# Optimization experiments

Measured on AMD Instinct MI355X. Metric: run time of the kernel, lower is better.

The kernel has to match this reference:

```python
import jax, jax.numpy as jnp
import numpy as np

B, S, D = 4, 2048, 1024
H, HK = 16, 4          # num_heads, num_heads_kv
HD = D // H            # head_dim = 64
G = H // HK            # kv groups = 4


def setup_inputs() -> dict:
    key = jax.random.key(0)
    ks = jax.random.split(key, 7)
    s = 0.02
    return {
        "query": jax.random.normal(ks[0], (B, S, D), jnp.float32),
        "key":   jax.random.normal(ks[1], (B, S, D), jnp.float32),
        "value": jax.random.normal(ks[2], (B, S, D), jnp.float32),
        # weights stored (in, out); equivalent to torch Linear y = x @ W.T
        "Wq": jax.random.normal(ks[3], (D, H * HD), jnp.float32) * s,
        "Wk": jax.random.normal(ks[4], (D, HK * HD), jnp.float32) * s,
        "Wv": jax.random.normal(ks[5], (D, HK * HD), jnp.float32) * s,
        "Wo": jax.random.normal(ks[6], (H * HD, D), jnp.float32) * s,
    }


def reference(query, key, value, Wq, Wk, Wv, Wo):
    b, qlen, _ = query.shape
    kvlen = key.shape[1]
    # projections
    q = (query @ Wq).reshape(b, qlen, H, HD)        # [b,q,H,hd]
    k = (key @ Wk).reshape(b, kvlen, HK, HD)        # [b,s,HK,hd]
    v = (value @ Wv).reshape(b, kvlen, HK, HD)      # [b,s,HK,hd]
    # GQA: q head h attends kv head h//G (repeat_interleave semantics)
    qg = q.reshape(b, qlen, HK, G, HD)              # head = kv*G + group
    scale = 1.0 / jnp.sqrt(jnp.asarray(HD, q.dtype))
    # scores [b,HK,G,q,s] -- broadcast kv heads, no materialized repeat
    scores = jnp.einsum('bqkgd,bskd->bkgqs', qg, k) * scale
    attn = jax.nn.softmax(scores, axis=-1)
    out = jnp.einsum('bkgqs,bskd->bqkgd', attn, v)  # [b,q,HK,G,hd]
    out = out.reshape(b, qlen, H * HD)
    return out @ Wo
```

## Files before the change

kernel.cpp:

```cpp
#include <hip/hip_runtime.h>


typedef unsigned short u16;
typedef unsigned int   u32;
typedef __bf16 bf16x4 __attribute__((ext_vector_type(4)));
typedef __bf16 bf16x8 __attribute__((ext_vector_type(8)));
typedef float  f32x4  __attribute__((ext_vector_type(4)));

#define MFMA(a,b,c) __builtin_amdgcn_mfma_f32_16x16x32_bf16((a),(b),(c),0,0,0)

#define GLDS(g, l) __builtin_amdgcn_global_load_lds(                          \
    (const __attribute__((address_space(1))) void*)(g),                       \
    (__attribute__((address_space(3))) void*)(l), 16, 0, 0)

#if __has_builtin(__builtin_amdgcn_exp2f)
#define EXP2(x) __builtin_amdgcn_exp2f(x)
#else
#define EXP2(x) exp2f(x)
#endif

__device__ __forceinline__ u16 f2bf(float f){
    u32 u = __builtin_bit_cast(u32, f);
    u += 0x7fffu + ((u >> 16) & 1u);
    return (u16)(u >> 16);
}
__device__ __forceinline__ u32 pk2(float a, float b){
#if __has_builtin(__builtin_amdgcn_cvt_pk_bf16_f32)
    auto r = __builtin_amdgcn_cvt_pk_bf16_f32(a, b);
    return __builtin_bit_cast(u32, r);
#else
    return (u32)f2bf(a) | ((u32)f2bf(b) << 16);
#endif
}
__device__ __forceinline__ bf16x8 ldfrag(const u16* p){
    return *(const bf16x8*)p;
}
__device__ __forceinline__ bf16x8 ld2x64(const u16* p){
    bf16x4 lo = *(const bf16x4*)p;
    bf16x4 hi = *(const bf16x4*)(p + 4);
    bf16x8 r;
    r[0]=lo[0]; r[1]=lo[1]; r[2]=lo[2]; r[3]=lo[3];
    r[4]=hi[0]; r[5]=hi[1]; r[6]=hi[2]; r[7]=hi[3];
    return r;
}

__global__ __launch_bounds__(256) void prep(const float* __restrict__ q,
                                            const float* __restrict__ k,
                                            const float* __restrict__ v,
                                            const float* __restrict__ Wq,
                                            const float* __restrict__ Wk,
                                            const float* __restrict__ Wv,
                                            const float* __restrict__ Wo,
                                            u16* Qc, u16* Kc, u16* Vc,
                                            u16* WqT, u16* WkT, u16* WvT, u16* WoT){
    const int tid = threadIdx.x, bid = blockIdx.x;
    if (bid < 2560){
        __shared__ float T[32][33];
        const float* W; u16* WT; int N, i;
        if (bid < 1024)      { W = Wq; WT = WqT; N = 1024; i = bid; }
        else if (bid < 1280) { W = Wk; WT = WkT; N =  256; i = bid - 1024; }
        else if (bid < 1536) { W = Wv; WT = WvT; N =  256; i = bid - 1280; }
        else                 { W = Wo; WT = WoT; N = 1024; i = bid - 1536; }
        int kt = (i & 31) * 32, nt = (i >> 5) * 32;
        int r = tid >> 3, c = tid & 7;
        float4 vv = *(const float4*)(W + (size_t)(kt + r) * N + nt + c * 4);
        T[r][c*4+0] = vv.x; T[r][c*4+1] = vv.y; T[r][c*4+2] = vv.z; T[r][c*4+3] = vv.w;
        __syncthreads();
        u32 lo = pk2(T[c*4+0][r], T[c*4+1][r]);
        u32 hi = pk2(T[c*4+2][r], T[c*4+3][r]);
        *(uint2*)(WT + (size_t)(nt + r) * 1024 + kt + c * 4) = make_uint2(lo, hi);
    } else {
        int i = bid - 2560;
        const float* src = (i < 512) ? q : (i < 1024 ? k : v);
        u16*         dst = (i < 512) ? Qc : (i < 1024 ? Kc : Vc);
        size_t off = (size_t)(i & 511) * 16384;
        const float* s = src + off;
        u16* d = dst + off;
        #pragma unroll
        for (int p = 0; p < 16; ++p){
            int idx = (p * 256 + tid) * 4;
            float4 vv = *(const float4*)(s + idx);
            *(uint2*)(d + idx) = make_uint2(pk2(vv.x, vv.y), pk2(vv.z, vv.w));
        }
    }
}

template<int EPI>
__device__ __forceinline__ void gemm_body(const u16* __restrict__ A,
                                          const u16* __restrict__ Bt,
                                          void* __restrict__ Cp,
                                          int N, int K, int m0, int n0,
                                          u16* As, u16* Bs, float oscale){
    const int tid  = threadIdx.x;
    const int wave = tid >> 6, lane = tid & 63;
    const int quad = lane >> 4, l15 = lane & 15;
    const int wm = wave >> 1, wn = wave & 1;
    const int srow = lane >> 3;
    const int scol = ((lane & 7) ^ srow) * 8;
    const int swz  = l15 & 7;

    f32x4 acc[4][4];
    #pragma unroll
    for (int i = 0; i < 4; ++i)
        #pragma unroll
        for (int j = 0; j < 4; ++j) acc[i][j] = (f32x4){0.f, 0.f, 0.f, 0.f};

    const int nkt = K >> 6;
    for (int kt = 0; kt < nkt; ++kt){
        __syncthreads();
        {
            const u16* ga = A + (size_t)(m0 + wave*32 + srow) * K + kt*64 + scol;
            u16* la = As + (wave*32) * 64;
            #pragma unroll
            for (int p = 0; p < 4; ++p)
                GLDS(ga + (size_t)(p*8) * K, la + p*8*64);
            const u16* gb = Bt + (size_t)(n0 + wave*32 + srow) * K + kt*64 + scol;
            u16* lb = Bs + (wave*32) * 64;
            #pragma unroll
            for (int p = 0; p < 4; ++p)
                GLDS(gb + (size_t)(p*8) * K, lb + p*8*64);
        }
        __syncthreads();
        #pragma unroll
        for (int ks = 0; ks < 2; ++ks){
            bf16x8 af[4], bfr[4];
            #pragma unroll
            for (int mt = 0; mt < 4; ++mt)
                af[mt] = ldfrag(&As[(wm*64 + mt*16 + l15) * 64 +
                                    (((ks*4 + quad) ^ swz) * 8)]);
            #pragma unroll
            for (int nt = 0; nt < 4; ++nt)
                bfr[nt] = ldfrag(&Bs[(wn*64 + nt*16 + l15) * 64 +
                                     (((ks*4 + quad) ^ swz) * 8)]);
            #pragma unroll
            for (int mt = 0; mt < 4; ++mt)
                #pragma unroll
                for (int nt = 0; nt < 4; ++nt){
                    if constexpr (EPI == 1)
                        acc[mt][nt] = MFMA(af[mt], bfr[nt], acc[mt][nt]);
                    else
                        acc[mt][nt] = MFMA(bfr[nt], af[mt], acc[mt][nt]);
                }
        }
    }
    #pragma unroll
    for (int mt = 0; mt < 4; ++mt){
        #pragma unroll
        for (int nt = 0; nt < 4; ++nt){
            if constexpr (EPI == 1){
                int rowb = m0 + wm*64 + mt*16 + quad*4;
                int col  = n0 + wn*64 + nt*16 + l15;
                u16* C = (u16*)Cp;
                int bb = rowb >> 11, s = rowb & 2047;
                u32 lo = pk2(acc[mt][nt][0], acc[mt][nt][1]);
                u32 hi = pk2(acc[mt][nt][2], acc[mt][nt][3]);
                *(uint2*)(C + (size_t)(bb * 256 + col) * 2048 + s) = make_uint2(lo, hi);
            } else {
                int row  = m0 + wm*64 + mt*16 + l15;
                int colb = n0 + wn*64 + nt*16 + quad*4;
                if constexpr (EPI == 0){
                    u16* C = (u16*)Cp;
                    u32 lo = pk2(acc[mt][nt][0]*oscale, acc[mt][nt][1]*oscale);
                    u32 hi = pk2(acc[mt][nt][2]*oscale, acc[mt][nt][3]*oscale);
                    *(uint2*)(C + (size_t)row * N + colb) = make_uint2(lo, hi);
                } else {
                    float* C = (float*)Cp;
                    *(f32x4*)(C + (size_t)row * N + colb) = acc[mt][nt];
                }
            }
        }
    }
}

__global__ __launch_bounds__(256) void gemm_qkv(const u16* Qc, const u16* WqT, u16* Qp,
                                                const u16* Kc, const u16* WkT, u16* Kp,
                                                const u16* Vc, const u16* WvT, u16* Vt,
                                                float qscale){
    __shared__ u16 As[128 * 64];
    __shared__ u16 Bs[128 * 64];
    int bid = blockIdx.x;
    if (bid < 512)
        gemm_body<0>(Qc, WqT, Qp, 1024, 1024, (bid >> 3) * 128, (bid & 7) * 128,
                     As, Bs, qscale);
    else if (bid < 640){
        int i = bid - 512;
        gemm_body<0>(Kc, WkT, Kp, 256, 1024, (i >> 1) * 128, (i & 1) * 128,
                     As, Bs, 1.0f);
    } else {
        int i = bid - 640;
        gemm_body<1>(Vc, WvT, Vt, 256, 1024, (i >> 1) * 128, (i & 1) * 128,
                     As, Bs, 1.0f);
    }
}

__global__ __launch_bounds__(256) void gemm_o(const u16* AO, const u16* WoT,
                                              float* Out){
    __shared__ u16 As[128 * 64];
    __shared__ u16 Bs[128 * 64];
    int bid = blockIdx.x;
    gemm_body<2>(AO, WoT, Out, 1024, 1024, (bid >> 3) * 128, (bid & 7) * 128,
                 As, Bs, 1.0f);
}

__global__ __launch_bounds__(512) void attn_k(const u16* __restrict__ Qp,
                                              const u16* __restrict__ Kp,
                                              const u16* __restrict__ Vt,
                                              u16* __restrict__ AO){
    constexpr int S = 2048, Dm = 1024, NKV = 256, PST = 88;
    __shared__ u16 Kb[2][64 * 64];
    __shared__ u16 Vb[2][64 * 64];
    __shared__ u16 Ps[128 * PST];
    const int tid = threadIdx.x, wave = tid >> 6, lane = tid & 63;
    const int quad = lane >> 4, l15 = lane & 15;
    const int qt = blockIdx.x, h = blockIdx.y, b = blockIdx.z;
    const int hk = h >> 2, q0 = qt * 128;
    u16* pw = Ps + wave * (16 * PST);

    const int srow = lane >> 3;
    const int scol = ((lane & 7) ^ srow) * 8;
    const int swz  = l15 & 7;

    auto issue = [&](int t){
        int j0 = t * 64, bufi = t & 1;
        int r = wave * 8 + srow;
        GLDS(Kp + (size_t)(b * S + j0 + r) * NKV + hk * 64 + scol,
             &Kb[bufi][wave * 8 * 64]);
        GLDS(Vt + (size_t)(b * NKV + hk * 64 + r) * S + j0 + scol,
             &Vb[bufi][wave * 8 * 64]);
    };

    issue(0);
    {
        int c8 = tid & 7, r0 = tid >> 3;
        #pragma unroll
        for (int p = 0; p < 2; ++p){
            int r = r0 + p * 64;
            uint4 v = *(const uint4*)(Qp + (size_t)(b * S + q0 + r) * Dm + h * 64 + c8 * 8);
            *(uint2*)&Ps[r * PST + c8 * 8]     = make_uint2(v.x, v.y);
            *(uint2*)&Ps[r * PST + c8 * 8 + 4] = make_uint2(v.z, v.w);
        }
    }
    __syncthreads();
    bf16x8 qf[2];
    #pragma unroll
    for (int ks = 0; ks < 2; ++ks)
        qf[ks] = ld2x64(&Ps[(wave*16 + l15) * PST + ks*32 + quad*8]);

    const u32 one2 = 0x3F803F80u;
    const bf16x8 ones = __builtin_bit_cast(bf16x8, make_uint4(one2, one2, one2, one2));

    f32x4 O[4];
    #pragma unroll
    for (int dt = 0; dt < 4; ++dt) O[dt] = (f32x4){0.f, 0.f, 0.f, 0.f};
    f32x4 sums = (f32x4){0.f, 0.f, 0.f, 0.f};

    for (int t = 0; t < 32; ++t){
        __syncthreads();
        if (t < 31) issue(t + 1);
        const u16* Kt = Kb[t & 1];
        const u16* Vs = Vb[t & 1];
        f32x4 sf[4];
        #pragma unroll
        for (int nt = 0; nt < 4; ++nt) sf[nt] = (f32x4){0.f, 0.f, 0.f, 0.f};
        #pragma unroll
        for (int ks = 0; ks < 2; ++ks){
            #pragma unroll
            for (int nt = 0; nt < 4; ++nt){
                bf16x8 ak = ldfrag(&Kt[(nt*16 + l15) * 64 + (((ks*4 + quad) ^ swz) * 8)]);
                sf[nt] = MFMA(ak, qf[ks], sf[nt]);
            }
        }
        #pragma unroll
        for (int nt = 0; nt < 4; ++nt){
            float e0 = EXP2(sf[nt][0]);
            float e1 = EXP2(sf[nt][1]);
            float e2 = EXP2(sf[nt][2]);
            float e3 = EXP2(sf[nt][3]);
            *(uint2*)&pw[l15 * PST + nt*16 + quad*4] =
                make_uint2(pk2(e0, e1), pk2(e2, e3));
        }
        __threadfence_block();
        #pragma unroll
        for (int ks = 0; ks < 2; ++ks){
            bf16x8 bp = ld2x64(&pw[l15 * PST + ks*32 + quad*8]);
            sums = MFMA(ones, bp, sums);
            #pragma unroll
            for (int dt = 0; dt < 4; ++dt){
                bf16x8 av = ldfrag(&Vs[(dt*16 + l15) * 64 + (((ks*4 + quad) ^ swz) * 8)]);
                O[dt] = MFMA(av, bp, O[dt]);
            }
        }
    }
    float inv = 1.0f / sums[0];
    size_t row = (size_t)(b * S + q0 + wave*16 + l15);
    #pragma unroll
    for (int dt = 0; dt < 4; ++dt){
        u32 lo = pk2(O[dt][0] * inv, O[dt][1] * inv);
        u32 hi = pk2(O[dt][2] * inv, O[dt][3] * inv);
        *(uint2*)(AO + row * Dm + h * 64 + dt*16 + quad*4) = make_uint2(lo, hi);
    }
}

extern "C" void kernel_launch(void* const* d_in, const int* in_sizes, int n_in,
                              void* d_out, int out_size, void* d_ws, size_t ws_size,
                              hipStream_t stream){
    const float* q  = (const float*)d_in[0];
    const float* k  = (const float*)d_in[1];
    const float* v  = (const float*)d_in[2];
    const float* Wq = (const float*)d_in[3];
    const float* Wk = (const float*)d_in[4];
    const float* Wv = (const float*)d_in[5];
    const float* Wo = (const float*)d_in[6];
    char* ws = (char*)d_ws;
    const size_t MB = 1u << 20;
    u16* WqT = (u16*)(ws);
    u16* WkT = (u16*)(ws + 2*MB);
    u16* WvT = (u16*)(ws + 2*MB + 512*1024);
    u16* WoT = (u16*)(ws + 3*MB);
    u16* Qc  = (u16*)(ws + 5*MB);
    u16* Kc  = (u16*)(ws + 21*MB);
    u16* Vc  = (u16*)(ws + 37*MB);
    u16* Qp  = (u16*)(ws + 53*MB);
    u16* Kp  = (u16*)(ws + 69*MB);
    u16* Vt  = (u16*)(ws + 73*MB);
    u16* AO  = (u16*)(ws + 5*MB);

    const float cexp = 0.125f * 1.44269504f;

    prep<<<dim3(4096), 256, 0, stream>>>(q, k, v, Wq, Wk, Wv, Wo,
                                         Qc, Kc, Vc, WqT, WkT, WvT, WoT);
    gemm_qkv<<<dim3(768), 256, 0, stream>>>(Qc, WqT, Qp, Kc, WkT, Kp,
                                            Vc, WvT, Vt, cexp);
    attn_k<<<dim3(16, 16, 4), 512, 0, stream>>>(Qp, Kp, Vt, AO);
    gemm_o<<<dim3(512), 256, 0, stream>>>(AO, WoT, (float*)d_out);
}
```

Before: 320.8 us.

## Give each attention wave four query row-tiles to reuse K/V fragments

```diff
diff --git a/kernel.cpp b/kernel.cpp
--- a/kernel.cpp
+++ b/kernel.cpp
@@ -202,19 +202,19 @@
                  As, Bs, 1.0f);
 }
 
-__global__ __launch_bounds__(512) void attn_k(const u16* __restrict__ Qp,
+__global__ __launch_bounds__(256) void attn_k(const u16* __restrict__ Qp,
                                               const u16* __restrict__ Kp,
                                               const u16* __restrict__ Vt,
                                               u16* __restrict__ AO){
-    constexpr int S = 2048, Dm = 1024, NKV = 256, PST = 88;
+    constexpr int S = 2048, Dm = 1024, NKV = 256, PST = 68;
     __shared__ u16 Kb[2][64 * 64];
     __shared__ u16 Vb[2][64 * 64];
-    __shared__ u16 Ps[128 * PST];
+    __shared__ u16 Ps[256 * PST];
     const int tid = threadIdx.x, wave = tid >> 6, lane = tid & 63;
     const int quad = lane >> 4, l15 = lane & 15;
-    const int qt = blockIdx.x, h = blockIdx.y, b = blockIdx.z;
-    const int hk = h >> 2, q0 = qt * 128;
-    u16* pw = Ps + wave * (16 * PST);
+    const int h = blockIdx.y, b = blockIdx.z;
+    const int hk = h >> 2, q0 = blockIdx.x * 256;
+    u16* pw = Ps + wave * (64 * PST);
 
     const int srow = lane >> 3;
     const int scol = ((lane & 7) ^ srow) * 8;
@@ -222,82 +222,108 @@
 
     auto issue = [&](int t){
         int j0 = t * 64, bufi = t & 1;
-        int r = wave * 8 + srow;
-        GLDS(Kp + (size_t)(b * S + j0 + r) * NKV + hk * 64 + scol,
-             &Kb[bufi][wave * 8 * 64]);
-        GLDS(Vt + (size_t)(b * NKV + hk * 64 + r) * S + j0 + scol,
-             &Vb[bufi][wave * 8 * 64]);
+        #pragma unroll
+        for (int p = 0; p < 2; ++p){
+            int r = wave * 16 + p * 8 + srow;
+            GLDS(Kp + (size_t)(b * S + j0 + r) * NKV + hk * 64 + scol,
+                 &Kb[bufi][(wave * 16 + p * 8) * 64]);
+            GLDS(Vt + (size_t)(b * NKV + hk * 64 + r) * S + j0 + scol,
+                 &Vb[bufi][(wave * 16 + p * 8) * 64]);
+        }
     };
 
     issue(0);
     {
         int c8 = tid & 7, r0 = tid >> 3;
         #pragma unroll
-        for (int p = 0; p < 2; ++p){
-            int r = r0 + p * 64;
+        for (int p = 0; p < 8; ++p){
+            int r = r0 + p * 32;
             uint4 v = *(const uint4*)(Qp + (size_t)(b * S + q0 + r) * Dm + h * 64 + c8 * 8);
             *(uint2*)&Ps[r * PST + c8 * 8]     = make_uint2(v.x, v.y);
             *(uint2*)&Ps[r * PST + c8 * 8 + 4] = make_uint2(v.z, v.w);
         }
     }
     __syncthreads();
-    bf16x8 qf[2];
-    #pragma unroll
-    for (int ks = 0; ks < 2; ++ks)
-        qf[ks] = ld2x64(&Ps[(wave*16 + l15) * PST + ks*32 + quad*8]);
+    bf16x8 qf[4][2];
+    #pragma unroll
+    for (int mt = 0; mt < 4; ++mt)
+        #pragma unroll
+        for (int ks = 0; ks < 2; ++ks)
+            qf[mt][ks] = ld2x64(&Ps[(wave*64 + mt*16 + l15) * PST + ks*32 + quad*8]);
 
     const u32 one2 = 0x3F803F80u;
     const bf16x8 ones = __builtin_bit_cast(bf16x8, make_uint4(one2, one2, one2, one2));
 
-    f32x4 O[4];
-    #pragma unroll
-    for (int dt = 0; dt < 4; ++dt) O[dt] = (f32x4){0.f, 0.f, 0.f, 0.f};
-    f32x4 sums = (f32x4){0.f, 0.f, 0.f, 0.f};
+    f32x4 O[4][4];
+    #pragma unroll
+    for (int dt = 0; dt < 4; ++dt)
+        #pragma unroll
+        for (int mt = 0; mt < 4; ++mt) O[dt][mt] = (f32x4){0.f, 0.f, 0.f, 0.f};
+    f32x4 sums[4];
+    #pragma unroll
+    for (int mt = 0; mt < 4; ++mt) sums[mt] = (f32x4){0.f, 0.f, 0.f, 0.f};
 
     for (int t = 0; t < 32; ++t){
         __syncthreads();
         if (t < 31) issue(t + 1);
         const u16* Kt = Kb[t & 1];
         const u16* Vs = Vb[t & 1];
-        f32x4 sf[4];
-        #pragma unroll
-        for (int nt = 0; nt < 4; ++nt) sf[nt] = (f32x4){0.f, 0.f, 0.f, 0.f};
+        bf16x8 ak[2][4];
+        #pragma unroll
+        for (int ks = 0; ks < 2; ++ks)
+            #pragma unroll
+            for (int nt = 0; nt < 4; ++nt)
+                ak[ks][nt] = ldfrag(&Kt[(nt*16 + l15) * 64 + (((ks*4 + quad) ^ swz) * 8)]);
+        #pragma unroll
+        for (int mt = 0; mt < 4; ++mt){
+            f32x4 sf[4];
+            #pragma unroll
+            for (int nt = 0; nt < 4; ++nt) sf[nt] = (f32x4){0.f, 0.f, 0.f, 0.f};
+            #pragma unroll
+            for (int ks = 0; ks < 2; ++ks)
+                #pragma unroll
+                for (int nt = 0; nt < 4; ++nt)
+                    sf[nt] = MFMA(ak[ks][nt], qf[mt][ks], sf[nt]);
+            #pragma unroll
+            for (int nt = 0; nt < 4; ++nt){
+                float e0 = EXP2(sf[nt][0]);
+                float e1 = EXP2(sf[nt][1]);
+                float e2 = EXP2(sf[nt][2]);
+                float e3 = EXP2(sf[nt][3]);
+                *(uint2*)&pw[(mt*16 + l15) * PST + nt*16 + quad*4] =
+                    make_uint2(pk2(e0, e1), pk2(e2, e3));
+            }
+        }
+        __threadfence_block();
         #pragma unroll
         for (int ks = 0; ks < 2; ++ks){
-            #pragma unroll
-            for (int nt = 0; nt < 4; ++nt){
-                bf16x8 ak = ldfrag(&Kt[(nt*16 + l15) * 64 + (((ks*4 + quad) ^ swz) * 8)]);
-                sf[nt] = MFMA(ak, qf[ks], sf[nt]);
-            }
-        }
-        #pragma unroll
-        for (int nt = 0; nt < 4; ++nt){
-            float e0 = EXP2(sf[nt][0]);
-            float e1 = EXP2(sf[nt][1]);
-            float e2 = EXP2(sf[nt][2]);
-            float e3 = EXP2(sf[nt][3]);
-            *(uint2*)&pw[l15 * PST + nt*16 + quad*4] =
-                make_uint2(pk2(e0, e1), pk2(e2, e3));
-        }
-        __threadfence_block();
-        #pragma unroll
-        for (int ks = 0; ks < 2; ++ks){
-            bf16x8 bp = ld2x64(&pw[l15 * PST + ks*32 + quad*8]);
-            sums = MFMA(ones, bp, sums);
-            #pragma unroll
-            for (int dt = 0; dt < 4; ++dt){
-                bf16x8 av = ldfrag(&Vs[(dt*16 + l15) * 64 + (((ks*4 + quad) ^ swz) * 8)]);
-                O[dt] = MFMA(av, bp, O[dt]);
-            }
-        }
-    }
-    float inv = 1.0f / sums[0];
-    size_t row = (size_t)(b * S + q0 + wave*16 + l15);
-    #pragma unroll
-    for (int dt = 0; dt < 4; ++dt){
-        u32 lo = pk2(O[dt][0] * inv, O[dt][1] * inv);
-        u32 hi = pk2(O[dt][2] * inv, O[dt][3] * inv);
-        *(uint2*)(AO + row * Dm + h * 64 + dt*16 + quad*4) = make_uint2(lo, hi);
+            bf16x8 av[4], bp[4];
+            #pragma unroll
+            for (int dt = 0; dt < 4; ++dt)
+                av[dt] = ldfrag(&Vs[(dt*16 + l15) * 64 + (((ks*4 + quad) ^ swz) * 8)]);
+            #pragma unroll
+            for (int mt = 0; mt < 4; ++mt)
+                bp[mt] = ld2x64(&pw[(mt*16 + l15) * PST + ks*32 + quad*8]);
+            #pragma unroll
+            for (int mt = 0; mt < 4; ++mt)
+                sums[mt] = MFMA(ones, bp[mt], sums[mt]);
+            #pragma unroll
+            for (int dt = 0; dt < 4; ++dt)
+                #pragma unroll
+                for (int mt = 0; mt < 4; ++mt)
+                    O[dt][mt] = MFMA(av[dt], bp[mt], O[dt][mt]);
+        }
+    }
+    #pragma unroll
+    for (int mt = 0; mt < 4; ++mt){
+        float inv = 1.0f / sums[mt][0];
+        size_t row = (size_t)(b * S + q0 + wave*64 + mt*16 + l15);
+        #pragma unroll
+        for (int dt = 0; dt < 4; ++dt){
+            u32 lo = pk2(O[dt][mt][0] * inv, O[dt][mt][1] * inv);
+            u32 hi = pk2(O[dt][mt][2] * inv, O[dt][mt][3] * inv);
+            *(uint2*)(AO + row * Dm + h * 64 + dt*16 + quad*4) = make_uint2(lo, hi);
+        }
     }
 }
 
@@ -331,6 +357,6 @@
                                          Qc, Kc, Vc, WqT, WkT, WvT, WoT);
     gemm_qkv<<<dim3(768), 256, 0, stream>>>(Qc, WqT, Qp, Kc, WkT, Kp,
                                             Vc, WvT, Vt, cexp);
-    attn_k<<<dim3(16, 16, 4), 512, 0, stream>>>(Qp, Kp, Vt, AO);
+    attn_k<<<dim3(8, 16, 4), 256, 0, stream>>>(Qp, Kp, Vt, AO);
     gemm_o<<<dim3(512), 256, 0, stream>>>(AO, WoT, (float*)d_out);
 }
```

New measurement: 367.6 us. 14.6% more time.
